# Optimization experiments

Hardware: AMD Instinct MI355X
Metric: run time of the kernel (lower is better)

The kernel has to match this reference:

```python
import jax, jax.numpy as jnp
import numpy as np

N_NODES = 50000


def spmm(rows, cols, vals, dense):
    # out[i,:] = sum_{e: rows[e]==i} vals[e] * dense[cols[e], :]
    gathered = dense[cols] * vals[:, None]  # [E, D]
    return jax.ops.segment_sum(gathered, rows, num_segments=N_NODES)


def setup_inputs() -> dict:
    key = jax.random.key(0)
    k1, k2, k3, k4, k5, k6 = jax.random.split(key, 6)
    N, E, F, H, C = N_NODES, 800000, 512, 256, 64
    node_features = jax.random.normal(k1, (N, F), dtype=jnp.float32)
    adj_rows = jax.random.randint(k2, (E,), 0, N, dtype=jnp.int32)
    adj_cols = jax.random.randint(k3, (E,), 0, N, dtype=jnp.int32)
    adj_vals = jax.random.uniform(k4, (E,), dtype=jnp.float32)
    W1 = jax.random.normal(k5, (F, H), dtype=jnp.float32) * (1.0 / np.sqrt(F))
    b1 = jnp.zeros((H,), dtype=jnp.float32)
    W2 = jax.random.normal(k6, (H, C), dtype=jnp.float32) * (1.0 / np.sqrt(H))
    b2 = jnp.zeros((C,), dtype=jnp.float32)
    return {"node_features": node_features, "adj_rows": adj_rows,
            "adj_cols": adj_cols, "adj_vals": adj_vals,
            "W1": W1, "b1": b1, "W2": W2, "b2": b2}


def reference(node_features, adj_rows, adj_cols, adj_vals, W1, b1, W2, b2):
    # Layer 1: dense projection then sparse aggregation, then ReLU.
    support1 = node_features @ W1 + b1           # [N, H]
    x = jax.nn.relu(spmm(adj_rows, adj_cols, adj_vals, support1))
    # Dropout is identity in eval mode (training=False).
    # Layer 2
    support2 = x @ W2 + b2                       # [N, C]
    x = spmm(adj_rows, adj_cols, adj_vals, support2)
    return jax.nn.log_softmax(x, axis=1)
```

## Files before the change

### kernel.cpp

```cpp
#include <hip/hip_runtime.h>

#define N_NODES 50000
#define N_EDGES 800000
#define F_IN    512
#define H_DIM   256
#define C_DIM   64
#define MPAD    50048

#define NB      196
#define NCHUNK  196
#define CHUNK   4096
#define BCAP    6144

typedef __bf16 bf16;
typedef __bf16 bf16x4 __attribute__((ext_vector_type(4)));
typedef __bf16 bf16x8 __attribute__((ext_vector_type(8)));
typedef float  f32x4  __attribute__((ext_vector_type(4)));
typedef unsigned int u32;
typedef unsigned long long u64;
typedef unsigned char u8;

__device__ __forceinline__ void gl_lds16(const void* g, void* l) {
    __builtin_amdgcn_global_load_lds(
        (const __attribute__((address_space(1))) u32*)g,
        (__attribute__((address_space(3))) u32*)l, 16, 0, 0);
}

__device__ __forceinline__ float unpack_val(u32 pk) {
    return __builtin_bit_cast(float, pk << 16);
}


__global__ __launch_bounds__(1024) void prep_k(const int* __restrict__ rows,
                                               const float* __restrict__ W1,
                                               const float* __restrict__ W2,
                                               u32* __restrict__ G,
                                               bf16* __restrict__ W1t,
                                               bf16* __restrict__ W2t) {
    __shared__ u32 h[16 * NB];
    int bid = blockIdx.x, tid = threadIdx.x;
    if (bid < NCHUNK) {
        int wid = tid >> 6;
        for (int i = tid; i < 16 * NB; i += 1024) h[i] = 0;
        __syncthreads();
        int base = bid * CHUNK;
        int end = base + CHUNK; if (end > N_EDGES) end = N_EDGES;
        for (int e = base + tid; e < end; e += 1024)
            atomicAdd(&h[wid * NB + (rows[e] >> 8)], 1);
        __syncthreads();
        if (tid < NB) {
            u32 s = 0;
#pragma unroll
            for (int w = 0; w < 16; w++) s += h[w * NB + tid];
            G[tid * NCHUNK + bid] = s;
        }
    } else {
        int i = (bid - NCHUNK) * 1024 + tid;
        if (i < F_IN * H_DIM) {
            int k = i >> 8, n = i & 255;
            W1t[n * F_IN + k] = (bf16)W1[i];
        } else {
            int j = i - F_IN * H_DIM;
            if (j < H_DIM * C_DIM) {
                int k = j >> 6, n = j & 63;
                W2t[n * H_DIM + k] = (bf16)W2[j];
            }
        }
    }
}


__global__ __launch_bounds__(512) void sg_k(const int* __restrict__ rows,
                                            const int* __restrict__ cols,
                                            const float* __restrict__ vals,
                                            const u32* __restrict__ G,
                                            u32* __restrict__ epack,
                                            u8* __restrict__ lrow,
                                            const float* __restrict__ A,
                                            const bf16* __restrict__ Bt,
                                            const float* __restrict__ bias,
                                            bf16* __restrict__ C) {
    __shared__ __attribute__((aligned(16))) char smem[49152];
    int bid = blockIdx.x, tid = threadIdx.x;
    int wid = tid >> 6, lane = tid & 63;

    if (bid < NCHUNK) {
        u32* cur = (u32*)smem;
        u32* wt  = (u32*)(smem + 1024);
        int c = bid;
        u32 tot = 0, pre = 0, incl = 0;
        if (tid < 256) {
            if (tid < NB) {
                for (int cc = 0; cc < NCHUNK; cc++) {
                    u32 v = G[tid * NCHUNK + cc];
                    tot += v;
                    if (cc < c) pre += v;
                }
            }
            incl = tot;
#pragma unroll
            for (int off = 1; off < 64; off <<= 1) {
                u32 u = __shfl_up(incl, off, 64);
                if (lane >= off) incl += u;
            }
            if (lane == 63) wt[wid] = incl;
        }
        __syncthreads();
        if (tid < 256) {
            u32 wpre = 0;
#pragma unroll
            for (int w = 0; w < 4; w++)
                if (w < wid) wpre += wt[w];
            if (tid < NB) cur[tid] = (wpre + incl - tot) + pre;
        }
        __syncthreads();
        int base = c * CHUNK;
        int end = base + CHUNK; if (end > N_EDGES) end = N_EDGES;
        for (int e = base + tid; e < end; e += 512) {
            int r = rows[e];
            unsigned short vb = __builtin_bit_cast(unsigned short, (bf16)vals[e]);
            u32 pk = ((u32)cols[e] << 16) | (u32)vb;
            u32 p = atomicAdd(&cur[r >> 8], 1);
            epack[p] = pk;
            lrow[p] = (u8)(r & 255);
        }
        return;
    }

    constexpr int BM = 128, BK = 64;
    bf16* As = (bf16*)smem;
    bf16* Bs = (bf16*)(smem + 16384);
    int wr = wid >> 2, wc = wid & 3;
    int l15 = lane & 15, hi = lane >> 4;
    int sw = l15 & 7;
    int bm = bid - NCHUNK;

    f32x4 acc[4][4];
#pragma unroll
    for (int m = 0; m < 4; m++)
#pragma unroll
        for (int n = 0; n < 4; n++) acc[m][n] = (f32x4){0.f, 0.f, 0.f, 0.f};

    for (int kt = 0; kt < F_IN; kt += BK) {
#pragma unroll
        for (int j = 0; j < 4; j++) {
            int ch = j * 512 + tid;
            int row = ch >> 3, kc = ch & 7;
            int kcs = kc ^ (row & 7);
            gl_lds16(Bt + (size_t)row * F_IN + kt + kcs * 8,
                     &Bs[(j * 512 + wid * 64) * 8]);
        }
#pragma unroll
        for (int j = 0; j < 2; j++) {
            int ch = j * 512 + tid;
            int row = ch >> 3, kc = ch & 7;
            int ar = bm * BM + row;
            if (ar >= N_NODES) ar = N_NODES - 1;
            const f32x4* src = (const f32x4*)(A + (size_t)ar * F_IN + kt + kc * 8);
            f32x4 u = src[0], v = src[1];
            bf16x8 o;
            o[0] = (bf16)u[0]; o[1] = (bf16)u[1]; o[2] = (bf16)u[2]; o[3] = (bf16)u[3];
            o[4] = (bf16)v[0]; o[5] = (bf16)v[1]; o[6] = (bf16)v[2]; o[7] = (bf16)v[3];
            *(bf16x8*)&As[row * BK + (kc ^ (row & 7)) * 8] = o;
        }
        __syncthreads();

        bf16x8 afr[2][4], bfr[2][4];
#pragma unroll
        for (int kk = 0; kk < 2; kk++) {
            int c = (kk * 4 + hi) ^ sw;
#pragma unroll
            for (int m = 0; m < 4; m++)
                afr[kk][m] = *(const bf16x8*)&As[(wr * 64 + m * 16 + l15) * BK + c * 8];
#pragma unroll
            for (int n = 0; n < 4; n++)
                bfr[kk][n] = *(const bf16x8*)&Bs[(wc * 64 + n * 16 + l15) * BK + c * 8];
        }
#pragma unroll
        for (int kk = 0; kk < 2; kk++)
#pragma unroll
            for (int m = 0; m < 4; m++)
#pragma unroll
                for (int n = 0; n < 4; n++)
                    acc[m][n] = __builtin_amdgcn_mfma_f32_16x16x32_bf16(
                        afr[kk][m], bfr[kk][n], acc[m][n], 0, 0, 0);
        __syncthreads();
    }

#pragma unroll
    for (int m = 0; m < 4; m++) {
        int row0 = bm * BM + wr * 64 + m * 16 + hi * 4;
#pragma unroll
        for (int n = 0; n < 4; n++) {
            int col = wc * 64 + n * 16 + l15;
            float bz = bias[col];
#pragma unroll
            for (int r = 0; r < 4; r++) {
                int row = row0 + r;
                if (row < N_NODES)
                    C[(size_t)row * H_DIM + col] = (bf16)(acc[m][n][r] + bz);
            }
        }
    }
}


__global__ __launch_bounds__(256) void sortC_k(u32* __restrict__ epack,
                                               const u8* __restrict__ lrow,
                                               const u32* __restrict__ G,
                                               int* __restrict__ starts) {
    __shared__ u32 edat[BCAP];
    __shared__ u32 sdat[BCAP];
    __shared__ u8  erow[BCAP];
    __shared__ u32 h[4 * 256];
    __shared__ u32 cur[256];
    __shared__ u32 wt1[4], wt2[4];
    __shared__ u32 sh_s, sh_n;
    int b = blockIdx.x, tid = threadIdx.x, wid = tid >> 6, lane = tid & 63;

    u32 btot = 0;
    if (tid < NB)
        for (int cc = 0; cc < NCHUNK; cc++) btot += G[tid * NCHUNK + cc];
    u32 bincl = btot;
#pragma unroll
    for (int off = 1; off < 64; off <<= 1) {
        u32 u = __shfl_up(bincl, off, 64);
        if (lane >= off) bincl += u;
    }
    if (lane == 63) wt1[wid] = bincl;
    __syncthreads();
    u32 bwpre = 0;
#pragma unroll
    for (int w = 0; w < 4; w++)
        if (w < wid) bwpre += wt1[w];
    if (tid == b) { sh_s = bwpre + bincl - btot; sh_n = btot; }
    __syncthreads();
    int s = (int)sh_s;
    int n = (int)sh_n;
    if (n > BCAP) n = BCAP;

    for (int i = tid; i < n; i += 256) { edat[i] = epack[s + i]; erow[i] = lrow[s + i]; }
    for (int i = tid; i < 1024; i += 256) h[i] = 0;
    __syncthreads();
    for (int i = tid; i < n; i += 256) atomicAdd(&h[wid * 256 + erow[i]], 1);
    __syncthreads();
    u32 tot = h[tid] + h[256 + tid] + h[512 + tid] + h[768 + tid];
    u32 incl = tot;
#pragma unroll
    for (int off = 1; off < 64; off <<= 1) {
        u32 u = __shfl_up(incl, off, 64);
        if (lane >= off) incl += u;
    }
    if (lane == 63) wt2[wid] = incl;
    __syncthreads();
    u32 wpre = 0;
#pragma unroll
    for (int w = 0; w < 4; w++)
        if (w < wid) wpre += wt2[w];
    u32 excl = wpre + incl - tot;
    cur[tid] = excl;
    int grow = b * 256 + tid;
    if (grow < N_NODES) starts[grow] = s + (int)excl;
    if (b == 0 && tid == 0) starts[N_NODES] = N_EDGES;
    __syncthreads();
    for (int i = tid; i < n; i += 256) {
        u32 p = atomicAdd(&cur[erow[i]], 1);
        sdat[p] = edat[i];
    }
    __syncthreads();
    for (int i = tid; i < n; i += 256) epack[s + i] = sdat[i];
}


__global__ __launch_bounds__(256) void gemm2_k(const bf16* __restrict__ A,
                                               const bf16* __restrict__ Bt,
                                               const float* __restrict__ bias,
                                               bf16* __restrict__ C) {
    constexpr int BM = 128, BK = 64;
    __shared__ bf16 As[BM * BK];
    __shared__ bf16 Bs[64 * BK];

    int tid = threadIdx.x;
    int wid = tid >> 6, lane = tid & 63;
    int wr = wid >> 1, wc = wid & 1;
    int l15 = lane & 15, hi = lane >> 4;
    int sw = l15 & 7;
    int bm = blockIdx.x;

    f32x4 acc[4][2];
#pragma unroll
    for (int m = 0; m < 4; m++)
#pragma unroll
        for (int n = 0; n < 2; n++) acc[m][n] = (f32x4){0.f, 0.f, 0.f, 0.f};

    for (int kt = 0; kt < H_DIM; kt += BK) {
#pragma unroll
        for (int j = 0; j < 4; j++) {
            int ch = j * 256 + tid;
            int row = ch >> 3, kc = ch & 7;
            int kcs = kc ^ (row & 7);
            gl_lds16(A + (size_t)(bm * BM + row) * H_DIM + kt + kcs * 8,
                     &As[(j * 256 + wid * 64) * 8]);
        }
#pragma unroll
        for (int j = 0; j < 2; j++) {
            int ch = j * 256 + tid;
            int row = ch >> 3, kc = ch & 7;
            int kcs = kc ^ (row & 7);
            gl_lds16(Bt + (size_t)row * H_DIM + kt + kcs * 8,
                     &Bs[(j * 256 + wid * 64) * 8]);
        }
        __syncthreads();

        bf16x8 afr[2][4], bfr[2][2];
#pragma unroll
        for (int kk = 0; kk < 2; kk++) {
            int c = (kk * 4 + hi) ^ sw;
#pragma unroll
            for (int m = 0; m < 4; m++)
                afr[kk][m] = *(const bf16x8*)&As[(wr * 64 + m * 16 + l15) * BK + c * 8];
#pragma unroll
            for (int n = 0; n < 2; n++)
                bfr[kk][n] = *(const bf16x8*)&Bs[(wc * 32 + n * 16 + l15) * BK + c * 8];
        }
#pragma unroll
        for (int kk = 0; kk < 2; kk++)
#pragma unroll
            for (int m = 0; m < 4; m++)
#pragma unroll
                for (int n = 0; n < 2; n++)
                    acc[m][n] = __builtin_amdgcn_mfma_f32_16x16x32_bf16(
                        afr[kk][m], bfr[kk][n], acc[m][n], 0, 0, 0);
        __syncthreads();
    }

#pragma unroll
    for (int m = 0; m < 4; m++) {
        int row0 = bm * BM + wr * 64 + m * 16 + hi * 4;
#pragma unroll
        for (int n = 0; n < 2; n++) {
            int col = wc * 32 + n * 16 + l15;
            float bz = bias[col];
#pragma unroll
            for (int r = 0; r < 4; r++) {
                int row = row0 + r;
                if (row < N_NODES)
                    C[(size_t)row * C_DIM + col] = (bf16)(acc[m][n][r] + bz);
            }
        }
    }
}


__global__ __launch_bounds__(256) void spmm1_k(const int* __restrict__ starts,
                                               const u32* __restrict__ epack,
                                               const bf16* __restrict__ s1,
                                               bf16* __restrict__ x16) {
    int wid = threadIdx.x >> 6, lane = threadIdx.x & 63;
    int row = blockIdx.x * 4 + wid;
    if (row >= N_NODES) return;
    int s = starts[row], e = starts[row + 1];
    f32x4 acc = (f32x4){0.f, 0.f, 0.f, 0.f};
    const bf16* s1l = s1 + lane * 4;
    int p = s;
    for (; p + 8 <= e; p += 8) {
        u32 k0 = __builtin_nontemporal_load(epack + p);
        u32 k1 = __builtin_nontemporal_load(epack + p + 1);
        u32 k2 = __builtin_nontemporal_load(epack + p + 2);
        u32 k3 = __builtin_nontemporal_load(epack + p + 3);
        u32 k4 = __builtin_nontemporal_load(epack + p + 4);
        u32 k5 = __builtin_nontemporal_load(epack + p + 5);
        u32 k6 = __builtin_nontemporal_load(epack + p + 6);
        u32 k7 = __builtin_nontemporal_load(epack + p + 7);
        bf16x4 g0 = *(const bf16x4*)(s1l + (size_t)(k0 >> 16) * H_DIM);
        bf16x4 g1 = *(const bf16x4*)(s1l + (size_t)(k1 >> 16) * H_DIM);
        bf16x4 g2 = *(const bf16x4*)(s1l + (size_t)(k2 >> 16) * H_DIM);
        bf16x4 g3 = *(const bf16x4*)(s1l + (size_t)(k3 >> 16) * H_DIM);
        bf16x4 g4 = *(const bf16x4*)(s1l + (size_t)(k4 >> 16) * H_DIM);
        bf16x4 g5 = *(const bf16x4*)(s1l + (size_t)(k5 >> 16) * H_DIM);
        bf16x4 g6 = *(const bf16x4*)(s1l + (size_t)(k6 >> 16) * H_DIM);
        bf16x4 g7 = *(const bf16x4*)(s1l + (size_t)(k7 >> 16) * H_DIM);
        float v0 = unpack_val(k0), v1 = unpack_val(k1), v2 = unpack_val(k2), v3 = unpack_val(k3);
        float v4 = unpack_val(k4), v5 = unpack_val(k5), v6 = unpack_val(k6), v7 = unpack_val(k7);
#pragma unroll
        for (int j = 0; j < 4; j++)
            acc[j] += v0 * (float)g0[j] + v1 * (float)g1[j] +
                      v2 * (float)g2[j] + v3 * (float)g3[j] +
                      v4 * (float)g4[j] + v5 * (float)g5[j] +
                      v6 * (float)g6[j] + v7 * (float)g7[j];
    }
    for (; p < e; ++p) {
        u32 k = __builtin_nontemporal_load(epack + p);
        float v = unpack_val(k);
        bf16x4 g = *(const bf16x4*)(s1l + (size_t)(k >> 16) * H_DIM);
#pragma unroll
        for (int j = 0; j < 4; j++) acc[j] += v * (float)g[j];
    }
    bf16x4 o;
#pragma unroll
    for (int j = 0; j < 4; j++) o[j] = (bf16)fmaxf(acc[j], 0.f);
    u64 bits = __builtin_bit_cast(u64, o);
    __builtin_nontemporal_store(bits, (u64*)(x16 + (size_t)row * H_DIM + lane * 4));
}


__global__ __launch_bounds__(256) void spmm2_sm_k(const int* __restrict__ starts,
                                                  const u32* __restrict__ epack,
                                                  const bf16* __restrict__ s2,
                                                  float* __restrict__ out) {
    int wid = threadIdx.x >> 6, lane = threadIdx.x & 63;
    int row = blockIdx.x * 4 + wid;
    if (row >= N_NODES) return;
    int s = starts[row], e = starts[row + 1];
    float acc = 0.f;
    int p = s;
    for (; p + 8 <= e; p += 8) {
        u32 k0 = __builtin_nontemporal_load(epack + p);
        u32 k1 = __builtin_nontemporal_load(epack + p + 1);
        u32 k2 = __builtin_nontemporal_load(epack + p + 2);
        u32 k3 = __builtin_nontemporal_load(epack + p + 3);
        u32 k4 = __builtin_nontemporal_load(epack + p + 4);
        u32 k5 = __builtin_nontemporal_load(epack + p + 5);
        u32 k6 = __builtin_nontemporal_load(epack + p + 6);
        u32 k7 = __builtin_nontemporal_load(epack + p + 7);
        float g0 = (float)s2[(size_t)(k0 >> 16) * C_DIM + lane];
        float g1 = (float)s2[(size_t)(k1 >> 16) * C_DIM + lane];
        float g2 = (float)s2[(size_t)(k2 >> 16) * C_DIM + lane];
        float g3 = (float)s2[(size_t)(k3 >> 16) * C_DIM + lane];
        float g4 = (float)s2[(size_t)(k4 >> 16) * C_DIM + lane];
        float g5 = (float)s2[(size_t)(k5 >> 16) * C_DIM + lane];
        float g6 = (float)s2[(size_t)(k6 >> 16) * C_DIM + lane];
        float g7 = (float)s2[(size_t)(k7 >> 16) * C_DIM + lane];
        acc += unpack_val(k0) * g0 + unpack_val(k1) * g1 +
               unpack_val(k2) * g2 + unpack_val(k3) * g3 +
               unpack_val(k4) * g4 + unpack_val(k5) * g5 +
               unpack_val(k6) * g6 + unpack_val(k7) * g7;
    }
    for (; p < e; ++p) {
        u32 k = __builtin_nontemporal_load(epack + p);
        acc += unpack_val(k) * (float)s2[(size_t)(k >> 16) * C_DIM + lane];
    }
    float mx = acc;
#pragma unroll
    for (int off = 32; off >= 1; off >>= 1) mx = fmaxf(mx, __shfl_xor(mx, off, 64));
    float ex = expf(acc - mx);
    float se = ex;
#pragma unroll
    for (int off = 32; off >= 1; off >>= 1) se += __shfl_xor(se, off, 64);
    __builtin_nontemporal_store((acc - mx) - logf(se),
                                out + (size_t)row * C_DIM + lane);
}


extern "C" void kernel_launch(void* const* d_in, const int* in_sizes, int n_in,
                              void* d_out, int out_size, void* d_ws, size_t ws_size,
                              hipStream_t stream) {
    const float* nf   = (const float*)d_in[0];
    const int*   rows = (const int*)d_in[1];
    const int*   cols = (const int*)d_in[2];
    const float* vals = (const float*)d_in[3];
    const float* W1   = (const float*)d_in[4];
    const float* b1   = (const float*)d_in[5];
    const float* W2   = (const float*)d_in[6];
    const float* b2   = (const float*)d_in[7];
    float* out = (float*)d_out;

    char* w = (char*)d_ws;
    auto alloc = [&](size_t b) { void* p = (void*)w; w += (b + 255) & ~(size_t)255; return p; };

    bf16* x16  = (bf16*)alloc((size_t)MPAD * H_DIM * 2);
    bf16* sup1 = (bf16*)alloc((size_t)N_NODES * H_DIM * 2);
    bf16* sup2 = sup1;
    bf16* W1t = (bf16*)alloc((size_t)H_DIM * F_IN * 2);
    bf16* W2t = (bf16*)alloc((size_t)C_DIM * H_DIM * 2);
    int* starts = (int*)alloc((size_t)(N_NODES + 1) * 4);
    u32* G      = (u32*)alloc((size_t)NB * NCHUNK * 4);
    u32* epack  = (u32*)alloc((size_t)N_EDGES * 4);
    u8*  lrow   = (u8*)alloc((size_t)N_EDGES);

    prep_k<<<NCHUNK + 144, 1024, 0, stream>>>(rows, W1, W2, G, W1t, W2t);
    sg_k<<<NCHUNK + MPAD / 128, 512, 0, stream>>>(rows, cols, vals, G, epack, lrow,
                                                  nf, W1t, b1, sup1);
    sortC_k<<<NB, 256, 0, stream>>>(epack, lrow, G, starts);
    spmm1_k<<<(N_NODES + 3) / 4, 256, 0, stream>>>(starts, epack, sup1, x16);
    gemm2_k<<<MPAD / 128, 256, 0, stream>>>(x16, W2t, b2, sup2);
    spmm2_sm_k<<<(N_NODES + 3) / 4, 256, 0, stream>>>(starts, epack, sup2, out);

    (void)in_sizes; (void)n_in; (void)out_size; (void)ws_size;
}
```

Before: 173.4 us.

## Locally sort edge chunk by bucket in LDS before coalesced global scatter

The scatter phase of the fused bucketing/GEMM kernel now builds a per-wave histogram in shared memory. It computes local bucket offsets with a block scan and places each edge into an LDS staging buffer sorted by bucket. The final writes to epack/lrow then go out in bucket-contiguous runs instead of random per-edge atomics on global positions, which should improve write coalescing. The cost is extra LDS traffic, more barriers and register arrays holding eight edges per thread.

```diff
diff --git a/kernel.cpp b/kernel.cpp
--- a/kernel.cpp
+++ b/kernel.cpp
@@ -85,9 +85,21 @@
     int wid = tid >> 6, lane = tid & 63;
 
     if (bid < NCHUNK) {
-        u32* cur = (u32*)smem;
-        u32* wt  = (u32*)(smem + 1024);
+        u32* sdat  = (u32*)smem;
+        u8*  sbkt  = (u8*)(smem + 16384);
+        u8*  srow  = (u8*)(smem + 20480);
+        u32* h     = (u32*)(smem + 24576);
+        u32* loff  = (u32*)(smem + 32768);
+        u32* lcur  = (u32*)(smem + 33792);
+        u32* gbase = (u32*)(smem + 34816);
+        u32* wt    = (u32*)(smem + 35840);
         int c = bid;
+        int base = c * CHUNK;
+        int end = base + CHUNK; if (end > N_EDGES) end = N_EDGES;
+        int n = end - base;
+
+        for (int i = tid; i < 2048; i += 512) h[i] = 0;
+
         u32 tot = 0, pre = 0, incl = 0;
         if (tid < 256) {
             if (tid < NB) {
@@ -111,18 +123,65 @@
 #pragma unroll
             for (int w = 0; w < 4; w++)
                 if (w < wid) wpre += wt[w];
-            if (tid < NB) cur[tid] = (wpre + incl - tot) + pre;
-        }
-        __syncthreads();
-        int base = c * CHUNK;
-        int end = base + CHUNK; if (end > N_EDGES) end = N_EDGES;
-        for (int e = base + tid; e < end; e += 512) {
-            int r = rows[e];
-            unsigned short vb = __builtin_bit_cast(unsigned short, (bf16)vals[e]);
-            u32 pk = ((u32)cols[e] << 16) | (u32)vb;
-            u32 p = atomicAdd(&cur[r >> 8], 1);
-            epack[p] = pk;
-            lrow[p] = (u8)(r & 255);
+            if (tid < NB) gbase[tid] = (wpre + incl - tot) + pre;
+        }
+
+        u32 pk_r[8], b_r[8], lr_r[8];
+#pragma unroll
+        for (int j = 0; j < 8; j++) {
+            int e = base + tid + j * 512;
+            bool ok = e < end;
+            int ee = ok ? e : base;
+            int r = rows[ee];
+            unsigned short vb = __builtin_bit_cast(unsigned short, (bf16)vals[ee]);
+            pk_r[j] = ((u32)cols[ee] << 16) | (u32)vb;
+            b_r[j] = (u32)(r >> 8);
+            lr_r[j] = (u32)(r & 255);
+            if (ok) atomicAdd(&h[wid * 256 + b_r[j]], 1);
+        }
+        __syncthreads();
+
+        u32 t2 = 0, incl2 = 0;
+        if (tid < 256) {
+#pragma unroll
+            for (int w2 = 0; w2 < 8; w2++) t2 += h[w2 * 256 + tid];
+            incl2 = t2;
+#pragma unroll
+            for (int off = 1; off < 64; off <<= 1) {
+                u32 u = __shfl_up(incl2, off, 64);
+                if (lane >= off) incl2 += u;
+            }
+            if (lane == 63) wt[wid] = incl2;
+        }
+        __syncthreads();
+        if (tid < 256) {
+            u32 wpre2 = 0;
+#pragma unroll
+            for (int w = 0; w < 4; w++)
+                if (w < wid) wpre2 += wt[w];
+            u32 excl = wpre2 + incl2 - t2;
+            loff[tid] = excl;
+            lcur[tid] = excl;
+        }
+        __syncthreads();
+
+#pragma unroll
+        for (int j = 0; j < 8; j++) {
+            int e = base + tid + j * 512;
+            if (e < end) {
+                u32 p = atomicAdd(&lcur[b_r[j]], 1);
+                sdat[p] = pk_r[j];
+                sbkt[p] = (u8)b_r[j];
+                srow[p] = (u8)lr_r[j];
+            }
+        }
+        __syncthreads();
+
+        for (int i = tid; i < n; i += 512) {
+            u32 b2 = sbkt[i];
+            u32 dst = gbase[b2] + (u32)i - loff[b2];
+            epack[dst] = sdat[i];
+            lrow[dst] = srow[i];
         }
         return;
     }
```

Result: no change. 172.3 us (-0.7%).
